# Kernel tuning notes

Measured on AMD Instinct MI355X. Metric: run time of the kernel, lower is better.

## Reference

```python
import jax, jax.numpy as jnp
import numpy as np

D_EDGE = 64


def segment_mean(feats, idx, num_segments):
    # feats: [E, d], idx: [E] int -> [num_segments, d] mean-aggregated
    s = jax.ops.segment_sum(feats, idx, num_segments=num_segments)
    cnt = jax.ops.segment_sum(jnp.ones((feats.shape[0],), feats.dtype), idx,
                              num_segments=num_segments)
    return s / jnp.maximum(cnt, 1.0)[:, None]


def setup_inputs() -> dict:
    key = jax.random.key(0)
    k1, k2, k3, k4, k5, k6 = jax.random.split(key, 6)
    N = 50000
    E = 800000
    Es = 400000
    edge_index = jax.random.randint(k1, (2, E), 0, N, dtype=jnp.int64 if jax.config.read('jax_enable_x64') else jnp.int32)
    same_frame_edge_index = jax.random.randint(k2, (2, Es), 0, N, dtype=edge_index.dtype)
    edge_attr = jax.random.normal(k3, (E, D_EDGE), dtype=jnp.float32)
    same_frame_edge_attr = jax.random.normal(k4, (Es, D_EDGE), dtype=jnp.float32)
    W1 = jax.random.normal(k5, (3 * D_EDGE, 128), dtype=jnp.float32) * (1.0 / np.sqrt(3 * D_EDGE))
    b1 = jnp.zeros((128,), jnp.float32)
    W2 = jax.random.normal(k6, (128, 64), dtype=jnp.float32) * (1.0 / np.sqrt(128))
    b2 = jnp.zeros((64,), jnp.float32)
    return {"edge_index": edge_index, "edge_attr": edge_attr, "num_nodes": N,
            "same_frame_edge_index": same_frame_edge_index,
            "same_frame_edge_attr": same_frame_edge_attr,
            "W1": W1, "b1": b1, "W2": W2, "b2": b2}


def reference(edge_index, edge_attr, num_nodes, same_frame_edge_index,
              same_frame_edge_attr, W1, b1, W2, b2):
    past_nodes, future_nodes = edge_index[0], edge_index[1]
    early, later = same_frame_edge_index[0], same_frame_edge_index[1]
    fwd_agg = segment_mean(edge_attr, future_nodes, num_nodes)   # [N, d]
    bwd_agg = segment_mean(edge_attr, past_nodes, num_nodes)     # [N, d]
    # vstack duplicates same-frame attrs; indices concat both directions
    sf_attr = jnp.concatenate([same_frame_edge_attr, same_frame_edge_attr], axis=0)
    sf_idx = jnp.concatenate([early, later], axis=0)
    frame_agg = segment_mean(sf_attr, sf_idx, num_nodes)         # [N, d]
    flow_total = jnp.concatenate([fwd_agg, frame_agg, bwd_agg], axis=1)  # [N, 3d]
    h = jax.nn.relu(flow_total @ W1 + b1)
    return h @ W2 + b2
```

## Files before the change

### kernel.cpp

```cpp
#include <hip/hip_runtime.h>
#include <hip/hip_bf16.h>
#include <cstdint>


#define D 64
#define R_BITS 6
#define R 64
#define CAP 2048
#define NB_MAX 4096
#define TILE_SRC 4096

typedef __attribute__((ext_vector_type(8))) short bf16x8;
typedef __attribute__((ext_vector_type(4))) float f32x4;

__device__ inline unsigned short f2bf(float x) {
    unsigned int u = __float_as_uint(x);
    unsigned int r = u + 0x7FFFu + ((u >> 16) & 1u);
    return (unsigned short)(r >> 16);
}

__global__ __launch_bounds__(256) void wconv_kernel(
    const float* __restrict__ W1, const float* __restrict__ W2,
    unsigned short* __restrict__ W1T, unsigned short* __restrict__ W2T)
{
    int i = blockIdx.x * 256 + threadIdx.x;
    if (i < 192 * 128) {
        int k = i >> 7, n = i & 127;
        W1T[n * 192 + k] = f2bf(W1[i]);
    }
    int j = i - 192 * 128;
    if (j >= 0 && j < 128 * 64) {
        int k = j >> 6, n = j & 63;
        W2T[n * 128 + k] = f2bf(W2[j]);
    }
}

__global__ __launch_bounds__(256) void bin_kernel(
    const int* __restrict__ ei, const int* __restrict__ sfi,
    int* __restrict__ bucket_cur, unsigned int* __restrict__ binned,
    int E, int Es, int N, int NB)
{
    __shared__ int hist[NB_MAX];
    __shared__ int base_sh[NB_MAX];

    int t = threadIdx.x;
    int tile0 = blockIdx.x * TILE_SRC;

    for (int b = t; b < NB; b += 256) hist[b] = 0;
    __syncthreads();

#pragma unroll
    for (int u = 0; u < 16; ++u) {
        int src = tile0 + u * 256 + t;
        if (src < E) {
            atomicAdd(&hist[((unsigned)ei[E + src]) >> R_BITS], 1);
            atomicAdd(&hist[((unsigned)(2 * N + ei[src])) >> R_BITS], 1);
        } else if (src < E + Es) {
            int e = src - E;
            atomicAdd(&hist[((unsigned)(N + sfi[e])) >> R_BITS], 1);
            atomicAdd(&hist[((unsigned)(N + sfi[Es + e])) >> R_BITS], 1);
        }
    }
    __syncthreads();

    for (int b = t; b < NB; b += 256) {
        int c = hist[b];
        base_sh[b] = (c > 0) ? atomicAdd(&bucket_cur[b], c) : 0;
        hist[b] = 0;
    }
    __syncthreads();

#pragma unroll
    for (int u = 0; u < 16; ++u) {
        int src = tile0 + u * 256 + t;
        if (src >= E + Es) continue;
        unsigned int g0, g1, e;
        if (src < E) {
            e = (unsigned)src;
            g0 = (unsigned)ei[E + src];
            g1 = (unsigned)(2 * N + ei[src]);
        } else {
            e = (unsigned)(src - E);
            g0 = (unsigned)(N + sfi[e]);
            g1 = (unsigned)(N + sfi[Es + e]);
        }
        int b0 = g0 >> R_BITS, b1 = g1 >> R_BITS;
        int r0 = base_sh[b0] + atomicAdd(&hist[b0], 1);
        if (r0 < CAP) binned[(size_t)b0 * CAP + r0] = ((g0 & (R - 1)) << 20) | e;
        int r1 = base_sh[b1] + atomicAdd(&hist[b1], 1);
        if (r1 < CAP) binned[(size_t)b1 * CAP + r1] = ((g1 & (R - 1)) << 20) | e;
    }
}

__global__ __launch_bounds__(256) void gather_sort_kernel(
    const float* __restrict__ edge_attr, const float* __restrict__ sf_attr,
    const unsigned int* __restrict__ binned, const int* __restrict__ bucket_cur,
    unsigned short* __restrict__ flow, int N, int T)
{
    __shared__ unsigned int stage[CAP];
    __shared__ unsigned int slist[CAP];
    __shared__ int kcnt[R];
    __shared__ int kstart[R];
    __shared__ int kcur[R];

    int b = blockIdx.x;
    int t = threadIdx.x;
    int w = t >> 6;
    int lane = t & 63;
    int slot = lane >> 4;
    int quad = lane & 15;

    if (t < R) kcnt[t] = 0;
    __syncthreads();

    int cb = bucket_cur[b];
    if (cb > CAP) cb = CAP;

    for (int i = t; i < cb; i += 256) {
        unsigned int p = binned[(size_t)b * CAP + i];
        stage[i] = p;
        atomicAdd(&kcnt[p >> 20], 1);
    }
    __syncthreads();

    if (t < R) {
        int c = kcnt[t];
        int v = c;
#pragma unroll
        for (int d = 1; d < 64; d <<= 1) {
            int x = __shfl_up(v, d);
            if (t >= d) v += x;
        }
        kstart[t] = v - c;
        kcur[t]   = v - c;
    }
    __syncthreads();

    for (int i = t; i < cb; i += 256) {
        unsigned int p = stage[i];
        int r = atomicAdd(&kcur[p >> 20], 1);
        slist[r] = p & 0xFFFFFu;
    }
    __syncthreads();

    for (int kk = w * 16; kk < w * 16 + 16; ++kk) {
        int g = (b << R_BITS) + kk;
        if (g >= T) break;
        int s = (g >= 2 * N) ? 2 : ((g >= N) ? 1 : 0);
        int node = g - s * N;
        const float4* attr4 =
            reinterpret_cast<const float4*>((s == 1) ? sf_attr : edge_attr);

        int start = kstart[kk];
        int deg   = kcnt[kk];
        int end   = start + deg;

        float ax = 0.f, ay = 0.f, az = 0.f, aw = 0.f;
        int k = start;
        for (; k + 16 <= end; k += 16) {
            unsigned int e0 = slist[k + slot];
            unsigned int e1 = slist[k + 4 + slot];
            unsigned int e2 = slist[k + 8 + slot];
            unsigned int e3 = slist[k + 12 + slot];
            float4 v0 = attr4[(size_t)e0 * 16 + quad];
            float4 v1 = attr4[(size_t)e1 * 16 + quad];
            float4 v2 = attr4[(size_t)e2 * 16 + quad];
            float4 v3 = attr4[(size_t)e3 * 16 + quad];
            ax += v0.x + v1.x + v2.x + v3.x;
            ay += v0.y + v1.y + v2.y + v3.y;
            az += v0.z + v1.z + v2.z + v3.z;
            aw += v0.w + v1.w + v2.w + v3.w;
        }
        for (; k + 8 <= end; k += 8) {
            unsigned int e0 = slist[k + slot];
            unsigned int e1 = slist[k + 4 + slot];
            float4 v0 = attr4[(size_t)e0 * 16 + quad];
            float4 v1 = attr4[(size_t)e1 * 16 + quad];
            ax += v0.x + v1.x; ay += v0.y + v1.y;
            az += v0.z + v1.z; aw += v0.w + v1.w;
        }
        if (k + 4 <= end) {
            unsigned int e0 = slist[k + slot];
            float4 v0 = attr4[(size_t)e0 * 16 + quad];
            ax += v0.x; ay += v0.y; az += v0.z; aw += v0.w;
            k += 4;
        }
        if (k + slot < end) {
            unsigned int e0 = slist[k + slot];
            float4 v0 = attr4[(size_t)e0 * 16 + quad];
            ax += v0.x; ay += v0.y; az += v0.z; aw += v0.w;
        }

        ax += __shfl_xor(ax, 16); ay += __shfl_xor(ay, 16);
        az += __shfl_xor(az, 16); aw += __shfl_xor(aw, 16);
        ax += __shfl_xor(ax, 32); ay += __shfl_xor(ay, 32);
        az += __shfl_xor(az, 32); aw += __shfl_xor(aw, 32);

        if (slot == 0) {
            float inv = 1.0f / fmaxf((float)deg, 1.0f);
            ushort4 o;
            o.x = f2bf(ax * inv);
            o.y = f2bf(ay * inv);
            o.z = f2bf(az * inv);
            o.w = f2bf(aw * inv);
            *reinterpret_cast<ushort4*>(
                &flow[(size_t)node * 192 + s * D + quad * 4]) = o;
        }
    }
}

#define MLP_NODES 64
#define FP 200
#define HP 136

__global__ __launch_bounds__(256) void mlp_kernel(
    const unsigned short* __restrict__ flow,
    const unsigned short* __restrict__ W1T,
    const float* __restrict__ b1,
    const unsigned short* __restrict__ W2T,
    const float* __restrict__ b2,
    float* __restrict__ out, int N)
{
    __shared__ unsigned short ldsf[MLP_NODES * FP];
    __shared__ unsigned short ldsh[MLP_NODES * HP];

    int t = threadIdx.x;
    int nbase = blockIdx.x * MLP_NODES;

    for (int i = t; i < 1536; i += 256) {
        int node = i / 24;
        int q    = i - node * 24;
        uint4 v = make_uint4(0u, 0u, 0u, 0u);
        if (nbase + node < N)
            v = *reinterpret_cast<const uint4*>(&flow[(size_t)(nbase + node) * 192 + q * 8]);
        *reinterpret_cast<uint4*>(&ldsf[node * FP + q * 8]) = v;
    }
    __syncthreads();

    int w   = t >> 6;
    int l   = t & 63;
    int m16 = l & 15;
    int kg  = l >> 4;

    f32x4 acc[8];
#pragma unroll
    for (int i = 0; i < 8; ++i) acc[i] = (f32x4){0.f, 0.f, 0.f, 0.f};

#pragma unroll
    for (int kt = 0; kt < 6; ++kt) {
        bf16x8 a = *reinterpret_cast<const bf16x8*>(
            &ldsf[(w * 16 + m16) * FP + kt * 32 + kg * 8]);
#pragma unroll
        for (int nt = 0; nt < 8; ++nt) {
            bf16x8 bfr = *reinterpret_cast<const bf16x8*>(
                &W1T[(size_t)(nt * 16 + m16) * 192 + kt * 32 + kg * 8]);
            acc[nt] = __builtin_amdgcn_mfma_f32_16x16x32_bf16(a, bfr, acc[nt], 0, 0, 0);
        }
    }

#pragma unroll
    for (int nt = 0; nt < 8; ++nt) {
        int col = nt * 16 + m16;
        float bias = b1[col];
#pragma unroll
        for (int r = 0; r < 4; ++r) {
            int node = w * 16 + kg * 4 + r;
            ldsh[node * HP + col] = f2bf(fmaxf(acc[nt][r] + bias, 0.f));
        }
    }
    __syncthreads();

    f32x4 acc2[4];
#pragma unroll
    for (int i = 0; i < 4; ++i) acc2[i] = (f32x4){0.f, 0.f, 0.f, 0.f};

#pragma unroll
    for (int kt = 0; kt < 4; ++kt) {
        bf16x8 a = *reinterpret_cast<const bf16x8*>(
            &ldsh[(w * 16 + m16) * HP + kt * 32 + kg * 8]);
#pragma unroll
        for (int nt = 0; nt < 4; ++nt) {
            bf16x8 bfr = *reinterpret_cast<const bf16x8*>(
                &W2T[(size_t)(nt * 16 + m16) * 128 + kt * 32 + kg * 8]);
            acc2[nt] = __builtin_amdgcn_mfma_f32_16x16x32_bf16(a, bfr, acc2[nt], 0, 0, 0);
        }
    }

#pragma unroll
    for (int nt = 0; nt < 4; ++nt) {
        int col = nt * 16 + m16;
        float bias = b2[col];
#pragma unroll
        for (int r = 0; r < 4; ++r) {
            int node = nbase + w * 16 + kg * 4 + r;
            if (node < N)
                out[(size_t)node * D + col] = acc2[nt][r] + bias;
        }
    }
}

extern "C" void kernel_launch(void* const* d_in, const int* in_sizes, int n_in,
                              void* d_out, int out_size, void* d_ws, size_t ws_size,
                              hipStream_t stream)
{
    const int*   edge_index = (const int*)d_in[0];
    const float* edge_attr  = (const float*)d_in[1];
    const int*   sf_index   = (const int*)d_in[3];
    const float* sf_attr    = (const float*)d_in[4];
    const float* W1         = (const float*)d_in[5];
    const float* b1         = (const float*)d_in[6];
    const float* W2         = (const float*)d_in[7];
    const float* b2         = (const float*)d_in[8];
    float* out = (float*)d_out;

    int E  = in_sizes[0] / 2;
    int Es = in_sizes[3] / 2;
    int N  = out_size / D;
    int T  = 3 * N;
    int NB = (T + R - 1) / R;

    unsigned short* flow = (unsigned short*)d_ws;
    size_t flow_elems = (size_t)N * 192;

    unsigned int* binned = (unsigned int*)(flow + flow_elems);
    int* bucket_cur = (int*)(binned + (size_t)NB * CAP);
    unsigned short* W1T = (unsigned short*)(bucket_cur + NB_MAX);
    unsigned short* W2T = W1T + 128 * 192;

    hipMemsetAsync(bucket_cur, 0, (size_t)NB * sizeof(int), stream);

    wconv_kernel<<<(192 * 128 + 128 * 64 + 255) / 256, 256, 0, stream>>>(
        W1, W2, W1T, W2T);

    int nsrc = E + Es;
    int bin_blocks = (nsrc + TILE_SRC - 1) / TILE_SRC;

    bin_kernel<<<bin_blocks, 256, 0, stream>>>(
        edge_index, sf_index, bucket_cur, binned, E, Es, N, NB);

    gather_sort_kernel<<<NB, 256, 0, stream>>>(
        edge_attr, sf_attr, binned, bucket_cur, flow, N, T);

    {
        int blocks = (N + MLP_NODES - 1) / MLP_NODES;
        mlp_kernel<<<blocks, 256, 0, stream>>>(flow, W1T, b1, W2T, b2, out, N);
    }
}
```

Measured before the change: 202.0 us.

## Replace per-bucket local sort with fixed-point LDS atomic accumulation

```diff
diff --git a/kernel.cpp b/kernel.cpp
--- a/kernel.cpp
+++ b/kernel.cpp
@@ -9,6 +9,8 @@
 #define CAP 2048
 #define NB_MAX 4096
 #define TILE_SRC 4096
+#define FXS 524288.0f
+#define FXSI (1.0f / 524288.0f)
 
 typedef __attribute__((ext_vector_type(8))) short bf16x8;
 typedef __attribute__((ext_vector_type(4))) float f32x4;
@@ -92,54 +94,53 @@
     }
 }
 
-__global__ __launch_bounds__(256) void gather_sort_kernel(
+__global__ __launch_bounds__(256) void bucket_accum_kernel(
     const float* __restrict__ edge_attr, const float* __restrict__ sf_attr,
     const unsigned int* __restrict__ binned, const int* __restrict__ bucket_cur,
     unsigned short* __restrict__ flow, int N, int T)
 {
-    __shared__ unsigned int stage[CAP];
-    __shared__ unsigned int slist[CAP];
+    __shared__ int acc[R * D];
     __shared__ int kcnt[R];
-    __shared__ int kstart[R];
-    __shared__ int kcur[R];
 
     int b = blockIdx.x;
     int t = threadIdx.x;
     int w = t >> 6;
-    int lane = t & 63;
-    int slot = lane >> 4;
-    int quad = lane & 15;
-
+    int j = t & 63;
+
+    for (int i = t; i < R * D; i += 256) acc[i] = 0;
     if (t < R) kcnt[t] = 0;
     __syncthreads();
 
     int cb = bucket_cur[b];
     if (cb > CAP) cb = CAP;
-
-    for (int i = t; i < cb; i += 256) {
-        unsigned int p = binned[(size_t)b * CAP + i];
-        stage[i] = p;
-        atomicAdd(&kcnt[p >> 20], 1);
-    }
-    __syncthreads();
-
-    if (t < R) {
-        int c = kcnt[t];
-        int v = c;
-#pragma unroll
-        for (int d = 1; d < 64; d <<= 1) {
-            int x = __shfl_up(v, d);
-            if (t >= d) v += x;
-        }
-        kstart[t] = v - c;
-        kcur[t]   = v - c;
-    }
-    __syncthreads();
-
-    for (int i = t; i < cb; i += 256) {
-        unsigned int p = stage[i];
-        int r = atomicAdd(&kcur[p >> 20], 1);
-        slist[r] = p & 0xFFFFFu;
+    const size_t base = (size_t)b * CAP;
+
+    for (int i0 = w * 8; i0 < cb; i0 += 32) {
+        int nm = cb - i0; if (nm > 8) nm = 8;
+        unsigned int p[8];
+#pragma unroll
+        for (int m = 0; m < 8; ++m)
+            if (m < nm) p[m] = binned[base + i0 + m];
+
+        int gl[8]; float v[8];
+#pragma unroll
+        for (int m = 0; m < 8; ++m) {
+            if (m < nm) {
+                gl[m] = (int)(p[m] >> 20);
+                unsigned int e = p[m] & 0xFFFFFu;
+                int g = (b << R_BITS) + gl[m];
+                const float* row = (g >= N && g < 2 * N)
+                    ? (sf_attr + (size_t)e * D) : (edge_attr + (size_t)e * D);
+                v[m] = row[j];
+            }
+        }
+#pragma unroll
+        for (int m = 0; m < 8; ++m) {
+            if (m < nm) {
+                atomicAdd(&acc[gl[m] * D + j], __float2int_rn(v[m] * FXS));
+                if (j == 0) atomicAdd(&kcnt[gl[m]], 1);
+            }
+        }
     }
     __syncthreads();
 
@@ -148,64 +149,8 @@
         if (g >= T) break;
         int s = (g >= 2 * N) ? 2 : ((g >= N) ? 1 : 0);
         int node = g - s * N;
-        const float4* attr4 =
-            reinterpret_cast<const float4*>((s == 1) ? sf_attr : edge_attr);
-
-        int start = kstart[kk];
-        int deg   = kcnt[kk];
-        int end   = start + deg;
-
-        float ax = 0.f, ay = 0.f, az = 0.f, aw = 0.f;
-        int k = start;
-        for (; k + 16 <= end; k += 16) {
-            unsigned int e0 = slist[k + slot];
-            unsigned int e1 = slist[k + 4 + slot];
-            unsigned int e2 = slist[k + 8 + slot];
-            unsigned int e3 = slist[k + 12 + slot];
-            float4 v0 = attr4[(size_t)e0 * 16 + quad];
-            float4 v1 = attr4[(size_t)e1 * 16 + quad];
-            float4 v2 = attr4[(size_t)e2 * 16 + quad];
-            float4 v3 = attr4[(size_t)e3 * 16 + quad];
-            ax += v0.x + v1.x + v2.x + v3.x;
-            ay += v0.y + v1.y + v2.y + v3.y;
-            az += v0.z + v1.z + v2.z + v3.z;
-            aw += v0.w + v1.w + v2.w + v3.w;
-        }
-        for (; k + 8 <= end; k += 8) {
-            unsigned int e0 = slist[k + slot];
-            unsigned int e1 = slist[k + 4 + slot];
-            float4 v0 = attr4[(size_t)e0 * 16 + quad];
-            float4 v1 = attr4[(size_t)e1 * 16 + quad];
-            ax += v0.x + v1.x; ay += v0.y + v1.y;
-            az += v0.z + v1.z; aw += v0.w + v1.w;
-        }
-        if (k + 4 <= end) {
-            unsigned int e0 = slist[k + slot];
-            float4 v0 = attr4[(size_t)e0 * 16 + quad];
-            ax += v0.x; ay += v0.y; az += v0.z; aw += v0.w;
-            k += 4;
-        }
-        if (k + slot < end) {
-            unsigned int e0 = slist[k + slot];
-            float4 v0 = attr4[(size_t)e0 * 16 + quad];
-            ax += v0.x; ay += v0.y; az += v0.z; aw += v0.w;
-        }
-
-        ax += __shfl_xor(ax, 16); ay += __shfl_xor(ay, 16);
-        az += __shfl_xor(az, 16); aw += __shfl_xor(aw, 16);
-        ax += __shfl_xor(ax, 32); ay += __shfl_xor(ay, 32);
-        az += __shfl_xor(az, 32); aw += __shfl_xor(aw, 32);
-
-        if (slot == 0) {
-            float inv = 1.0f / fmaxf((float)deg, 1.0f);
-            ushort4 o;
-            o.x = f2bf(ax * inv);
-            o.y = f2bf(ay * inv);
-            o.z = f2bf(az * inv);
-            o.w = f2bf(aw * inv);
-            *reinterpret_cast<ushort4*>(
-                &flow[(size_t)node * 192 + s * D + quad * 4]) = o;
-        }
+        float inv = FXSI / fmaxf((float)kcnt[kk], 1.0f);
+        flow[(size_t)node * 192 + s * D + j] = f2bf((float)acc[kk * D + j] * inv);
     }
 }
 
@@ -338,7 +283,7 @@
     bin_kernel<<<bin_blocks, 256, 0, stream>>>(
         edge_index, sf_index, bucket_cur, binned, E, Es, N, NB);
 
-    gather_sort_kernel<<<NB, 256, 0, stream>>>(
+    bucket_accum_kernel<<<NB, 256, 0, stream>>>(
         edge_attr, sf_attr, binned, bucket_cur, flow, N, T);
 
     {
```

After: 380.1 us. 1.88x slower.
